# Kernel tuning notes

Measured on AMD Instinct MI355X. Metric: run time of the kernel, lower is better.

The kernel has to match this reference:

```python
import jax, jax.numpy as jnp
from jax import lax
import numpy as np

B, T, D, H, O = 256, 512, 512, 1024, 512

def setup_inputs() -> dict:
    key = jax.random.key(0)
    k1, k2, k3, k4 = jax.random.split(key, 4)
    return {
        "x": jax.random.normal(k1, (B, T, D), dtype=jnp.float32),
        "h0": jnp.zeros((B, H), dtype=jnp.float32),
        "w_xh": jax.random.normal(k2, (D, H), dtype=jnp.float32) * 0.05,
        "w_hh": jax.random.normal(k3, (H, H), dtype=jnp.float32) * 0.05,
        "w_hy": jax.random.normal(k4, (H, O), dtype=jnp.float32) * 0.05,
    }

def reference(x, h0, w_xh, w_hh, w_hy):
    # x: [B, T, D] -> scan over time. Each step matches MyRNNCell.call:
    #   h' = tanh(x_t @ W_xh + h @ W_hh);  y_t = h' @ W_hy
    xT = jnp.swapaxes(x, 0, 1)  # [T, B, D]
    def step(h, xt):
        h_next = jnp.tanh(xt @ w_xh + h @ w_hh)  # [B, H]
        return h_next, h_next @ w_hy             # output [B, O]
    h_final, outs = lax.scan(step, h0, xT)
    return jnp.swapaxes(outs, 0, 1), h_final  # [B, T, O], [B, H]
```

## Files before the change

kernel.cpp:

```cpp
#include <hip/hip_runtime.h>
#include <hip/hip_bf16.h>

#define BB 256
#define TT 512
#define DD 512
#define HH 1024
#define OO 512

typedef unsigned short u16;
typedef unsigned int u32;
typedef unsigned long long u64;
typedef __attribute__((ext_vector_type(8))) short frag8;
typedef __attribute__((ext_vector_type(4))) float floatx4;

#define MFMA16 __builtin_amdgcn_mfma_f32_16x16x32_bf16

__device__ __forceinline__ u16 f2b(float f) {
  union { float f; u32 u; } v; v.f = f;
  u32 r = v.u + 0x7fffu + ((v.u >> 16) & 1u);
  return (u16)(r >> 16);
}
__device__ __forceinline__ float b2f(u16 b) {
  union { u32 u; float f; } v; v.u = ((u32)b) << 16; return v.f;
}
__device__ __forceinline__ float fast_tanh(float x) {
  float e = __expf(2.0f * x);
  return 1.0f - 2.0f / (e + 1.0f);
}
__device__ __forceinline__ frag8 mkfrag(u64 lo, u64 hi) {
  union { u64 d[2]; frag8 f; } u; u.d[0] = lo; u.d[1] = hi; return u.f;
}

__global__ void k_transpose(const float* __restrict__ src, u16* __restrict__ dst,
                            int K, int N) {
  int idx = blockIdx.x * 256 + threadIdx.x;
  if (idx >= K * N) return;
  int k = idx / N, n = idx - k * N;
  dst[(u64)n * K + k] = f2b(src[idx]);
}

__global__ void k_init_s0(const float* __restrict__ h0, u16* __restrict__ S) {
  int idx = blockIdx.x * 256 + threadIdx.x;
  if (idx < BB * HH) S[idx] = f2b(h0[idx]);
}

__global__ void k_final_h(const u16* __restrict__ Sl, float* __restrict__ out) {
  int idx = blockIdx.x * 256 + threadIdx.x;
  if (idx < BB * HH) out[idx] = b2f(Sl[idx]);
}

__global__ void k_zero_flags(int* __restrict__ flags, int n) {
  int idx = blockIdx.x * 256 + threadIdx.x;
  if (idx < n) flags[idx] = 0;
}

__global__ __launch_bounds__(256) void k_gemm_xh(const float* __restrict__ X,
                                                 const u16* __restrict__ Wt,
                                                 u16* __restrict__ S) {
  __shared__ __align__(16) u16 As[64 * 72];
  __shared__ __align__(16) u16 Bs[64 * 72];
  const int tid = threadIdx.x;
  const int m0 = blockIdx.x * 64, n0 = blockIdx.y * 64;
  const int lane = tid & 63, wv = tid >> 6;
  const int fr = lane & 15, quad = lane >> 4;

  floatx4 acc[4];
#pragma unroll
  for (int i = 0; i < 4; ++i) acc[i] = (floatx4){0.f, 0.f, 0.f, 0.f};

  for (int kc = 0; kc < DD; kc += 64) {
    const float* Ab = X + (u64)m0 * DD + kc;
#pragma unroll
    for (int it = 0; it < 4; ++it) {
      int linear = (it * 256 + tid) * 4;
      int r = linear >> 6, c = linear & 63;
      float4 v = *(const float4*)(Ab + (u64)r * DD + c);
      ushort4 o;
      o.x = f2b(v.x); o.y = f2b(v.y); o.z = f2b(v.z); o.w = f2b(v.w);
      *(ushort4*)&As[r * 72 + c] = o;
    }
    const u16* Bb = Wt + (u64)n0 * DD + kc;
#pragma unroll
    for (int it = 0; it < 2; ++it) {
      int linear = (it * 256 + tid) * 8;
      int n = linear >> 6, c = linear & 63;
      *(uint4*)&Bs[n * 72 + c] = *(const uint4*)(Bb + (u64)n * DD + c);
    }
    __syncthreads();
#pragma unroll
    for (int kk = 0; kk < 64; kk += 32) {
      frag8 bf = *(const frag8*)&Bs[(wv * 16 + fr) * 72 + kk + quad * 8];
#pragma unroll
      for (int i = 0; i < 4; ++i) {
        frag8 af = *(const frag8*)&As[(i * 16 + fr) * 72 + kk + quad * 8];
        acc[i] = MFMA16(af, bf, acc[i], 0, 0, 0);
      }
    }
    __syncthreads();
  }
  const int col = n0 + wv * 16 + fr;
#pragma unroll
  for (int i = 0; i < 4; ++i) {
#pragma unroll
    for (int r = 0; r < 4; ++r) {
      int m = m0 + i * 16 + quad * 4 + r;
      int t = m & (TT - 1);
      int b = m >> 9;
      S[((u64)(t + 1) * BB + b) * HH + col] = f2b(acc[i][r]);
    }
  }
}

__global__ __launch_bounds__(256) void k_scan(const u16* __restrict__ Whh_t,
                                              u16* __restrict__ S,
                                              int* __restrict__ flags) {
  extern __shared__ __align__(16) u16 smem[];
  u16* Ws = smem;
  float* Red = (float*)(smem + 32 * 1032);

  const int tid = threadIdx.x;
  const int mb = blockIdx.x;
  const int nb = blockIdx.y;
  const int m0 = mb * 32, n0 = nb * 32;
  const int lane = tid & 63, wv = tid >> 6;
  const int fr = lane & 15, q = lane >> 4;
  const int kbase = wv * 256;
  const int er = tid >> 4;
  const int ec = (tid & 15) * 2;

  {
    const u16* Wb = Whh_t + (u64)n0 * HH;
#pragma unroll
    for (int it = 0; it < 16; ++it) {
      int linear = (it * 256 + tid) * 8;
      int r = linear >> 10, c = linear & 1023;
      *(uint4*)&Ws[r * 1032 + c] = *(const uint4*)(Wb + (u64)r * HH + c);
    }
  }
  __syncthreads();

  for (int t = 0; t < TT; ++t) {
    u16* Sout = S + (u64)(t + 1) * BB * HH + (u64)m0 * HH + n0;

    u32 z01 = *(const u32*)(Sout + (u64)er * HH + ec);
    u32 z23 = *(const u32*)(Sout + (u64)(er + 16) * HH + ec);
    asm volatile("" :: "v"(z01), "v"(z23));

    if (t > 0) {
      int* fb = flags + ((u64)(t - 1) * 8 + mb) * 32;
      if (lane < 8) {
        while (__hip_atomic_load(&fb[wv * 8 + lane], __ATOMIC_RELAXED,
                                 __HIP_MEMORY_SCOPE_AGENT) == 0) {
          __builtin_amdgcn_s_sleep(2);
        }
      }
      __builtin_amdgcn_fence(__ATOMIC_ACQUIRE, "workgroup");
    }

    const u16* St = S + (u64)t * BB * HH;
    const u64* A0p = (const u64*)(St + (u64)(m0 + fr) * HH + kbase + q * 8);
    const u64* A1p = (const u64*)(St + (u64)(m0 + 16 + fr) * HH + kbase + q * 8);
    u64 a0[16], a1[16];
#pragma unroll
    for (int kt = 0; kt < 8; ++kt) {
      a0[2 * kt]     = __hip_atomic_load(A0p + kt * 8,     __ATOMIC_RELAXED, __HIP_MEMORY_SCOPE_AGENT);
      a0[2 * kt + 1] = __hip_atomic_load(A0p + kt * 8 + 1, __ATOMIC_RELAXED, __HIP_MEMORY_SCOPE_AGENT);
      a1[2 * kt]     = __hip_atomic_load(A1p + kt * 8,     __ATOMIC_RELAXED, __HIP_MEMORY_SCOPE_AGENT);
      a1[2 * kt + 1] = __hip_atomic_load(A1p + kt * 8 + 1, __ATOMIC_RELAXED, __HIP_MEMORY_SCOPE_AGENT);
    }

    floatx4 acc[2][2];
#pragma unroll
    for (int i = 0; i < 2; ++i)
#pragma unroll
      for (int j = 0; j < 2; ++j) acc[i][j] = (floatx4){0.f, 0.f, 0.f, 0.f};

#pragma unroll
    for (int kt = 0; kt < 8; ++kt) {
      const int k = kbase + kt * 32 + q * 8;
      frag8 b0 = *(const frag8*)&Ws[fr * 1032 + k];
      frag8 b1 = *(const frag8*)&Ws[(16 + fr) * 1032 + k];
      frag8 af0 = mkfrag(a0[2 * kt], a0[2 * kt + 1]);
      frag8 af1 = mkfrag(a1[2 * kt], a1[2 * kt + 1]);
      acc[0][0] = MFMA16(af0, b0, acc[0][0], 0, 0, 0);
      acc[0][1] = MFMA16(af0, b1, acc[0][1], 0, 0, 0);
      acc[1][0] = MFMA16(af1, b0, acc[1][0], 0, 0, 0);
      acc[1][1] = MFMA16(af1, b1, acc[1][1], 0, 0, 0);
    }

#pragma unroll
    for (int im = 0; im < 2; ++im)
#pragma unroll
      for (int in = 0; in < 2; ++in)
#pragma unroll
        for (int r = 0; r < 4; ++r) {
          int row = im * 16 + q * 4 + r;
          int col = in * 16 + fr;
          Red[((u64)wv * 32 + row) * 33 + col] = acc[im][in][r];
        }
    __syncthreads();

    float s00 = Red[(0 * 32 + er) * 33 + ec]     + Red[(1 * 32 + er) * 33 + ec] +
                Red[(2 * 32 + er) * 33 + ec]     + Red[(3 * 32 + er) * 33 + ec];
    float s01 = Red[(0 * 32 + er) * 33 + ec + 1] + Red[(1 * 32 + er) * 33 + ec + 1] +
                Red[(2 * 32 + er) * 33 + ec + 1] + Red[(3 * 32 + er) * 33 + ec + 1];
    float s10 = Red[(0 * 32 + er + 16) * 33 + ec]     + Red[(1 * 32 + er + 16) * 33 + ec] +
                Red[(2 * 32 + er + 16) * 33 + ec]     + Red[(3 * 32 + er + 16) * 33 + ec];
    float s11 = Red[(0 * 32 + er + 16) * 33 + ec + 1] + Red[(1 * 32 + er + 16) * 33 + ec + 1] +
                Red[(2 * 32 + er + 16) * 33 + ec + 1] + Red[(3 * 32 + er + 16) * 33 + ec + 1];
    float z0 = b2f((u16)(z01 & 0xffffu)), z1 = b2f((u16)(z01 >> 16));
    float z2 = b2f((u16)(z23 & 0xffffu)), z3 = b2f((u16)(z23 >> 16));
    u32 p0 = (u32)f2b(fast_tanh(s00 + z0)) | ((u32)f2b(fast_tanh(s01 + z1)) << 16);
    u32 p1 = (u32)f2b(fast_tanh(s10 + z2)) | ((u32)f2b(fast_tanh(s11 + z3)) << 16);
    __hip_atomic_store((u32*)(Sout + (u64)er * HH + ec), p0,
                       __ATOMIC_RELAXED, __HIP_MEMORY_SCOPE_AGENT);
    __hip_atomic_store((u32*)(Sout + (u64)(er + 16) * HH + ec), p1,
                       __ATOMIC_RELAXED, __HIP_MEMORY_SCOPE_AGENT);
    __syncthreads();

    if (tid == 0) {
      __hip_atomic_store(&flags[((u64)t * 8 + mb) * 32 + nb], 1,
                         __ATOMIC_RELAXED, __HIP_MEMORY_SCOPE_AGENT);
    }
  }
}

__global__ __launch_bounds__(256) void k_gemm_hy(const u16* __restrict__ Hs,
                                                 const u16* __restrict__ Wt,
                                                 float* __restrict__ out) {
  __shared__ __align__(16) u16 As[64 * 72];
  __shared__ __align__(16) u16 Bs[64 * 72];
  const int tid = threadIdx.x;
  const int m0 = blockIdx.x * 64, n0 = blockIdx.y * 64;
  const int lane = tid & 63, wv = tid >> 6;
  const int fr = lane & 15, quad = lane >> 4;

  floatx4 acc[4];
#pragma unroll
  for (int i = 0; i < 4; ++i) acc[i] = (floatx4){0.f, 0.f, 0.f, 0.f};

  for (int kc = 0; kc < HH; kc += 64) {
    const u16* Ab = Hs + (u64)m0 * HH + kc;
#pragma unroll
    for (int it = 0; it < 2; ++it) {
      int linear = (it * 256 + tid) * 8;
      int r = linear >> 6, c = linear & 63;
      *(uint4*)&As[r * 72 + c] = *(const uint4*)(Ab + (u64)r * HH + c);
    }
    const u16* Bb = Wt + (u64)n0 * HH + kc;
#pragma unroll
    for (int it = 0; it < 2; ++it) {
      int linear = (it * 256 + tid) * 8;
      int n = linear >> 6, c = linear & 63;
      *(uint4*)&Bs[n * 72 + c] = *(const uint4*)(Bb + (u64)n * HH + c);
    }
    __syncthreads();
#pragma unroll
    for (int kk = 0; kk < 64; kk += 32) {
      frag8 bf = *(const frag8*)&Bs[(wv * 16 + fr) * 72 + kk + quad * 8];
#pragma unroll
      for (int i = 0; i < 4; ++i) {
        frag8 af = *(const frag8*)&As[(i * 16 + fr) * 72 + kk + quad * 8];
        acc[i] = MFMA16(af, bf, acc[i], 0, 0, 0);
      }
    }
    __syncthreads();
  }
  const int col = n0 + wv * 16 + fr;
#pragma unroll
  for (int i = 0; i < 4; ++i) {
#pragma unroll
    for (int r = 0; r < 4; ++r) {
      int m = m0 + i * 16 + quad * 4 + r;
      int t = m >> 8;
      int b = m & (BB - 1);
      out[(u64)b * (TT * OO) + (u64)t * OO + col] = acc[i][r];
    }
  }
}

extern "C" void kernel_launch(void* const* d_in, const int* in_sizes, int n_in,
                              void* d_out, int out_size, void* d_ws, size_t ws_size,
                              hipStream_t stream) {
  (void)in_sizes; (void)n_in; (void)out_size; (void)ws_size;
  const float* x    = (const float*)d_in[0];
  const float* h0   = (const float*)d_in[1];
  const float* w_xh = (const float*)d_in[2];
  const float* w_hh = (const float*)d_in[3];
  const float* w_hy = (const float*)d_in[4];
  float* out = (float*)d_out;

  u16* S = (u16*)d_ws;
  u64 s_elems = (u64)(TT + 1) * BB * HH;
  u16* Wxh_t = S + s_elems;
  u16* Whh_t = Wxh_t + (u64)HH * DD;
  u16* Why_t = Whh_t + (u64)HH * HH;
  int* flags = (int*)Wxh_t;
  const int n_flags = TT * 8 * 32;

  k_transpose<<<dim3((DD * HH + 255) / 256), dim3(256), 0, stream>>>(w_xh, Wxh_t, DD, HH);
  k_transpose<<<dim3((HH * HH + 255) / 256), dim3(256), 0, stream>>>(w_hh, Whh_t, HH, HH);
  k_transpose<<<dim3((HH * OO + 255) / 256), dim3(256), 0, stream>>>(w_hy, Why_t, HH, OO);
  k_init_s0<<<dim3(BB * HH / 256), dim3(256), 0, stream>>>(h0, S);

  k_gemm_xh<<<dim3((BB * TT) / 64, HH / 64), dim3(256), 0, stream>>>(x, Wxh_t, S);

  k_zero_flags<<<dim3((n_flags + 255) / 256), dim3(256), 0, stream>>>(flags, n_flags);

  const int scan_lds = 32 * 1032 * 2 + 4 * 32 * 33 * 4;
  hipFuncSetAttribute((const void*)k_scan,
                      hipFuncAttributeMaxDynamicSharedMemorySize, scan_lds);
  k_scan<<<dim3(8, 32), dim3(256), scan_lds, stream>>>(Whh_t, S, flags);

  k_gemm_hy<<<dim3((TT * BB) / 64, OO / 64), dim3(256), 0, stream>>>(
      S + (u64)BB * HH, Why_t, out);
  k_final_h<<<dim3(BB * HH / 256), dim3(256), 0, stream>>>(
      S + (u64)TT * BB * HH, out + (u64)BB * TT * OO);
}
```

Baseline: 3.964 ms.

## Fuse input projection into scan and replace flags with sentinel-value polling

Removes the separate x@W_xh GEMM and computes each step's input projection inside the persistent scan kernel, with W_xh slices held in LDS, so the xh projection no longer round-trips through the state buffer. The per-block flag array, its zeroing kernel and the second barrier are replaced by filling the state buffer with an all-ones sentinel and spinning on the data itself until no sentinel words remain. The reduction buffer is double-buffered to drop the trailing syncthreads, and packed bf16 conversion is used. This adds more LDS use and per-step reads of x inside the serial loop, and relies on a tanh output never encoding as the 0xFFFF sentinel pattern.

```diff
diff --git a/kernel.cpp b/kernel.cpp
--- a/kernel.cpp
+++ b/kernel.cpp
@@ -14,6 +14,8 @@
 typedef __attribute__((ext_vector_type(4))) float floatx4;
 
 #define MFMA16 __builtin_amdgcn_mfma_f32_16x16x32_bf16
+#define AL(p) __hip_atomic_load((p), __ATOMIC_RELAXED, __HIP_MEMORY_SCOPE_AGENT)
+#define AS(p, v) __hip_atomic_store((p), (v), __ATOMIC_RELAXED, __HIP_MEMORY_SCOPE_AGENT)
 
 __device__ __forceinline__ u16 f2b(float f) {
   union { float f; u32 u; } v; v.f = f;
@@ -29,6 +31,17 @@
 }
 __device__ __forceinline__ frag8 mkfrag(u64 lo, u64 hi) {
   union { u64 d[2]; frag8 f; } u; u.d[0] = lo; u.d[1] = hi; return u.f;
+}
+__device__ __forceinline__ u32 cvtpk(float lo, float hi) {
+  u32 r;
+  asm("v_cvt_pk_bf16_f32 %0, %1, %2" : "=v"(r) : "v"(lo), "v"(hi));
+  return r;
+}
+__device__ __forceinline__ frag8 cvt8(float4 a, float4 b) {
+  union { u32 w[4]; frag8 f; } u;
+  u.w[0] = cvtpk(a.x, a.y); u.w[1] = cvtpk(a.z, a.w);
+  u.w[2] = cvtpk(b.x, b.y); u.w[3] = cvtpk(b.z, b.w);
+  return u.f;
 }
 
 __global__ void k_transpose(const float* __restrict__ src, u16* __restrict__ dst,
@@ -49,74 +62,19 @@
   if (idx < BB * HH) out[idx] = b2f(Sl[idx]);
 }
 
-__global__ void k_zero_flags(int* __restrict__ flags, int n) {
-  int idx = blockIdx.x * 256 + threadIdx.x;
-  if (idx < n) flags[idx] = 0;
-}
-
-__global__ __launch_bounds__(256) void k_gemm_xh(const float* __restrict__ X,
-                                                 const u16* __restrict__ Wt,
-                                                 u16* __restrict__ S) {
-  __shared__ __align__(16) u16 As[64 * 72];
-  __shared__ __align__(16) u16 Bs[64 * 72];
-  const int tid = threadIdx.x;
-  const int m0 = blockIdx.x * 64, n0 = blockIdx.y * 64;
-  const int lane = tid & 63, wv = tid >> 6;
-  const int fr = lane & 15, quad = lane >> 4;
-
-  floatx4 acc[4];
-#pragma unroll
-  for (int i = 0; i < 4; ++i) acc[i] = (floatx4){0.f, 0.f, 0.f, 0.f};
-
-  for (int kc = 0; kc < DD; kc += 64) {
-    const float* Ab = X + (u64)m0 * DD + kc;
-#pragma unroll
-    for (int it = 0; it < 4; ++it) {
-      int linear = (it * 256 + tid) * 4;
-      int r = linear >> 6, c = linear & 63;
-      float4 v = *(const float4*)(Ab + (u64)r * DD + c);
-      ushort4 o;
-      o.x = f2b(v.x); o.y = f2b(v.y); o.z = f2b(v.z); o.w = f2b(v.w);
-      *(ushort4*)&As[r * 72 + c] = o;
-    }
-    const u16* Bb = Wt + (u64)n0 * DD + kc;
-#pragma unroll
-    for (int it = 0; it < 2; ++it) {
-      int linear = (it * 256 + tid) * 8;
-      int n = linear >> 6, c = linear & 63;
-      *(uint4*)&Bs[n * 72 + c] = *(const uint4*)(Bb + (u64)n * DD + c);
-    }
-    __syncthreads();
-#pragma unroll
-    for (int kk = 0; kk < 64; kk += 32) {
-      frag8 bf = *(const frag8*)&Bs[(wv * 16 + fr) * 72 + kk + quad * 8];
-#pragma unroll
-      for (int i = 0; i < 4; ++i) {
-        frag8 af = *(const frag8*)&As[(i * 16 + fr) * 72 + kk + quad * 8];
-        acc[i] = MFMA16(af, bf, acc[i], 0, 0, 0);
-      }
-    }
-    __syncthreads();
-  }
-  const int col = n0 + wv * 16 + fr;
-#pragma unroll
-  for (int i = 0; i < 4; ++i) {
-#pragma unroll
-    for (int r = 0; r < 4; ++r) {
-      int m = m0 + i * 16 + quad * 4 + r;
-      int t = m & (TT - 1);
-      int b = m >> 9;
-      S[((u64)(t + 1) * BB + b) * HH + col] = f2b(acc[i][r]);
-    }
-  }
+__global__ void k_fill_sent(uint4* __restrict__ p) {
+  u64 i = (u64)blockIdx.x * 256 + threadIdx.x;
+  p[i] = make_uint4(0xFFFFFFFFu, 0xFFFFFFFFu, 0xFFFFFFFFu, 0xFFFFFFFFu);
 }
 
 __global__ __launch_bounds__(256) void k_scan(const u16* __restrict__ Whh_t,
-                                              u16* __restrict__ S,
-                                              int* __restrict__ flags) {
+                                              const u16* __restrict__ Wxh_t,
+                                              const float* __restrict__ X,
+                                              u16* __restrict__ S) {
   extern __shared__ __align__(16) u16 smem[];
   u16* Ws = smem;
-  float* Red = (float*)(smem + 32 * 1032);
+  u16* Wxs = smem + 32 * 1032;
+  float* Red = (float*)(smem + 32 * 1032 + 32 * 520);
 
   const int tid = threadIdx.x;
   const int mb = blockIdx.x;
@@ -125,6 +83,7 @@
   const int lane = tid & 63, wv = tid >> 6;
   const int fr = lane & 15, q = lane >> 4;
   const int kbase = wv * 256;
+  const int xkbase = wv * 128;
   const int er = tid >> 4;
   const int ec = (tid & 15) * 2;
 
@@ -137,57 +96,75 @@
       *(uint4*)&Ws[r * 1032 + c] = *(const uint4*)(Wb + (u64)r * HH + c);
     }
   }
+  {
+    const u16* Wb = Wxh_t + (u64)n0 * DD;
+#pragma unroll
+    for (int it = 0; it < 8; ++it) {
+      int linear = (it * 256 + tid) * 8;
+      int r = linear >> 9, c = linear & 511;
+      *(uint4*)&Wxs[r * 520 + c] = *(const uint4*)(Wb + (u64)r * DD + c);
+    }
+  }
   __syncthreads();
 
   for (int t = 0; t < TT; ++t) {
-    u16* Sout = S + (u64)(t + 1) * BB * HH + (u64)m0 * HH + n0;
-
-    u32 z01 = *(const u32*)(Sout + (u64)er * HH + ec);
-    u32 z23 = *(const u32*)(Sout + (u64)(er + 16) * HH + ec);
-    asm volatile("" :: "v"(z01), "v"(z23));
-
-    if (t > 0) {
-      int* fb = flags + ((u64)(t - 1) * 8 + mb) * 32;
-      if (lane < 8) {
-        while (__hip_atomic_load(&fb[wv * 8 + lane], __ATOMIC_RELAXED,
-                                 __HIP_MEMORY_SCOPE_AGENT) == 0) {
-          __builtin_amdgcn_s_sleep(2);
-        }
-      }
-      __builtin_amdgcn_fence(__ATOMIC_ACQUIRE, "workgroup");
+    const float* xr0 = X + ((u64)(m0 + fr) * TT + t) * DD + xkbase;
+    const float* xr1 = X + ((u64)(m0 + 16 + fr) * TT + t) * DD + xkbase;
+    float4 xv[16];
+#pragma unroll
+    for (int xkt = 0; xkt < 4; ++xkt) {
+      xv[xkt * 4 + 0] = *(const float4*)(xr0 + xkt * 32 + q * 8);
+      xv[xkt * 4 + 1] = *(const float4*)(xr0 + xkt * 32 + q * 8 + 4);
+      xv[xkt * 4 + 2] = *(const float4*)(xr1 + xkt * 32 + q * 8);
+      xv[xkt * 4 + 3] = *(const float4*)(xr1 + xkt * 32 + q * 8 + 4);
+    }
+
+    floatx4 acc[2][2];
+#pragma unroll
+    for (int i = 0; i < 2; ++i)
+#pragma unroll
+      for (int j = 0; j < 2; ++j) acc[i][j] = (floatx4){0.f, 0.f, 0.f, 0.f};
+
+#pragma unroll
+    for (int xkt = 0; xkt < 4; ++xkt) {
+      const int k = xkbase + xkt * 32 + q * 8;
+      frag8 ax0 = cvt8(xv[xkt * 4 + 0], xv[xkt * 4 + 1]);
+      frag8 ax1 = cvt8(xv[xkt * 4 + 2], xv[xkt * 4 + 3]);
+      frag8 b0 = *(const frag8*)&Wxs[fr * 520 + k];
+      frag8 b1 = *(const frag8*)&Wxs[(16 + fr) * 520 + k];
+      acc[0][0] = MFMA16(ax0, b0, acc[0][0], 0, 0, 0);
+      acc[0][1] = MFMA16(ax0, b1, acc[0][1], 0, 0, 0);
+      acc[1][0] = MFMA16(ax1, b0, acc[1][0], 0, 0, 0);
+      acc[1][1] = MFMA16(ax1, b1, acc[1][1], 0, 0, 0);
     }
 
     const u16* St = S + (u64)t * BB * HH;
     const u64* A0p = (const u64*)(St + (u64)(m0 + fr) * HH + kbase + q * 8);
     const u64* A1p = (const u64*)(St + (u64)(m0 + 16 + fr) * HH + kbase + q * 8);
-    u64 a0[16], a1[16];
 #pragma unroll
     for (int kt = 0; kt < 8; ++kt) {
-      a0[2 * kt]     = __hip_atomic_load(A0p + kt * 8,     __ATOMIC_RELAXED, __HIP_MEMORY_SCOPE_AGENT);
-      a0[2 * kt + 1] = __hip_atomic_load(A0p + kt * 8 + 1, __ATOMIC_RELAXED, __HIP_MEMORY_SCOPE_AGENT);
-      a1[2 * kt]     = __hip_atomic_load(A1p + kt * 8,     __ATOMIC_RELAXED, __HIP_MEMORY_SCOPE_AGENT);
-      a1[2 * kt + 1] = __hip_atomic_load(A1p + kt * 8 + 1, __ATOMIC_RELAXED, __HIP_MEMORY_SCOPE_AGENT);
-    }
-
-    floatx4 acc[2][2];
-#pragma unroll
-    for (int i = 0; i < 2; ++i)
-#pragma unroll
-      for (int j = 0; j < 2; ++j) acc[i][j] = (floatx4){0.f, 0.f, 0.f, 0.f};
-
-#pragma unroll
-    for (int kt = 0; kt < 8; ++kt) {
+      u64 c0, c1, c2, c3;
+      for (;;) {
+        c0 = AL(A0p + kt * 8);     c1 = AL(A0p + kt * 8 + 1);
+        c2 = AL(A1p + kt * 8);     c3 = AL(A1p + kt * 8 + 1);
+        u32 bad = ((u32)c0 == 0xFFFFFFFFu) | ((u32)(c0 >> 32) == 0xFFFFFFFFu) |
+                  ((u32)c1 == 0xFFFFFFFFu) | ((u32)(c1 >> 32) == 0xFFFFFFFFu) |
+                  ((u32)c2 == 0xFFFFFFFFu) | ((u32)(c2 >> 32) == 0xFFFFFFFFu) |
+                  ((u32)c3 == 0xFFFFFFFFu) | ((u32)(c3 >> 32) == 0xFFFFFFFFu);
+        if (!bad) break;
+      }
       const int k = kbase + kt * 32 + q * 8;
       frag8 b0 = *(const frag8*)&Ws[fr * 1032 + k];
       frag8 b1 = *(const frag8*)&Ws[(16 + fr) * 1032 + k];
-      frag8 af0 = mkfrag(a0[2 * kt], a0[2 * kt + 1]);
-      frag8 af1 = mkfrag(a1[2 * kt], a1[2 * kt + 1]);
+      frag8 af0 = mkfrag(c0, c1);
+      frag8 af1 = mkfrag(c2, c3);
       acc[0][0] = MFMA16(af0, b0, acc[0][0], 0, 0, 0);
       acc[0][1] = MFMA16(af0, b1, acc[0][1], 0, 0, 0);
       acc[1][0] = MFMA16(af1, b0, acc[1][0], 0, 0, 0);
       acc[1][1] = MFMA16(af1, b1, acc[1][1], 0, 0, 0);
     }
 
+    float* R = Red + (t & 1) * (4 * 32 * 33);
 #pragma unroll
     for (int im = 0; im < 2; ++im)
 #pragma unroll
@@ -196,32 +173,23 @@
         for (int r = 0; r < 4; ++r) {
           int row = im * 16 + q * 4 + r;
           int col = in * 16 + fr;
-          Red[((u64)wv * 32 + row) * 33 + col] = acc[im][in][r];
+          R[(wv * 32 + row) * 33 + col] = acc[im][in][r];
         }
     __syncthreads();
 
-    float s00 = Red[(0 * 32 + er) * 33 + ec]     + Red[(1 * 32 + er) * 33 + ec] +
-                Red[(2 * 32 + er) * 33 + ec]     + Red[(3 * 32 + er) * 33 + ec];
-    float s01 = Red[(0 * 32 + er) * 33 + ec + 1] + Red[(1 * 32 + er) * 33 + ec + 1] +
-                Red[(2 * 32 + er) * 33 + ec + 1] + Red[(3 * 32 + er) * 33 + ec + 1];
-    float s10 = Red[(0 * 32 + er + 16) * 33 + ec]     + Red[(1 * 32 + er + 16) * 33 + ec] +
-                Red[(2 * 32 + er + 16) * 33 + ec]     + Red[(3 * 32 + er + 16) * 33 + ec];
-    float s11 = Red[(0 * 32 + er + 16) * 33 + ec + 1] + Red[(1 * 32 + er + 16) * 33 + ec + 1] +
-                Red[(2 * 32 + er + 16) * 33 + ec + 1] + Red[(3 * 32 + er + 16) * 33 + ec + 1];
-    float z0 = b2f((u16)(z01 & 0xffffu)), z1 = b2f((u16)(z01 >> 16));
-    float z2 = b2f((u16)(z23 & 0xffffu)), z3 = b2f((u16)(z23 >> 16));
-    u32 p0 = (u32)f2b(fast_tanh(s00 + z0)) | ((u32)f2b(fast_tanh(s01 + z1)) << 16);
-    u32 p1 = (u32)f2b(fast_tanh(s10 + z2)) | ((u32)f2b(fast_tanh(s11 + z3)) << 16);
-    __hip_atomic_store((u32*)(Sout + (u64)er * HH + ec), p0,
-                       __ATOMIC_RELAXED, __HIP_MEMORY_SCOPE_AGENT);
-    __hip_atomic_store((u32*)(Sout + (u64)(er + 16) * HH + ec), p1,
-                       __ATOMIC_RELAXED, __HIP_MEMORY_SCOPE_AGENT);
-    __syncthreads();
-
-    if (tid == 0) {
-      __hip_atomic_store(&flags[((u64)t * 8 + mb) * 32 + nb], 1,
-                         __ATOMIC_RELAXED, __HIP_MEMORY_SCOPE_AGENT);
-    }
+    u16* Sout = S + (u64)(t + 1) * BB * HH + (u64)m0 * HH + n0;
+    float s00 = R[(0 * 32 + er) * 33 + ec]     + R[(1 * 32 + er) * 33 + ec] +
+                R[(2 * 32 + er) * 33 + ec]     + R[(3 * 32 + er) * 33 + ec];
+    float s01 = R[(0 * 32 + er) * 33 + ec + 1] + R[(1 * 32 + er) * 33 + ec + 1] +
+                R[(2 * 32 + er) * 33 + ec + 1] + R[(3 * 32 + er) * 33 + ec + 1];
+    float s10 = R[(0 * 32 + er + 16) * 33 + ec]     + R[(1 * 32 + er + 16) * 33 + ec] +
+                R[(2 * 32 + er + 16) * 33 + ec]     + R[(3 * 32 + er + 16) * 33 + ec];
+    float s11 = R[(0 * 32 + er + 16) * 33 + ec + 1] + R[(1 * 32 + er + 16) * 33 + ec + 1] +
+                R[(2 * 32 + er + 16) * 33 + ec + 1] + R[(3 * 32 + er + 16) * 33 + ec + 1];
+    u32 p0 = cvtpk(fast_tanh(s00), fast_tanh(s01));
+    u32 p1 = cvtpk(fast_tanh(s10), fast_tanh(s11));
+    AS((u32*)(Sout + (u64)er * HH + ec), p0);
+    AS((u32*)(Sout + (u64)(er + 16) * HH + ec), p1);
   }
 }
 
@@ -295,22 +263,19 @@
   u16* Wxh_t = S + s_elems;
   u16* Whh_t = Wxh_t + (u64)HH * DD;
   u16* Why_t = Whh_t + (u64)HH * HH;
-  int* flags = (int*)Wxh_t;
-  const int n_flags = TT * 8 * 32;
 
   k_transpose<<<dim3((DD * HH + 255) / 256), dim3(256), 0, stream>>>(w_xh, Wxh_t, DD, HH);
   k_transpose<<<dim3((HH * HH + 255) / 256), dim3(256), 0, stream>>>(w_hh, Whh_t, HH, HH);
   k_transpose<<<dim3((HH * OO + 255) / 256), dim3(256), 0, stream>>>(w_hy, Why_t, HH, OO);
   k_init_s0<<<dim3(BB * HH / 256), dim3(256), 0, stream>>>(h0, S);
 
-  k_gemm_xh<<<dim3((BB * TT) / 64, HH / 64), dim3(256), 0, stream>>>(x, Wxh_t, S);
-
-  k_zero_flags<<<dim3((n_flags + 255) / 256), dim3(256), 0, stream>>>(flags, n_flags);
-
-  const int scan_lds = 32 * 1032 * 2 + 4 * 32 * 33 * 4;
+  k_fill_sent<<<dim3(65536), dim3(256), 0, stream>>>(
+      (uint4*)(S + (u64)BB * HH));
+
+  const int scan_lds = 32 * 1032 * 2 + 32 * 520 * 2 + 2 * 4 * 32 * 33 * 4;
   hipFuncSetAttribute((const void*)k_scan,
                       hipFuncAttributeMaxDynamicSharedMemorySize, scan_lds);
-  k_scan<<<dim3(8, 32), dim3(256), scan_lds, stream>>>(Whh_t, S, flags);
+  k_scan<<<dim3(8, 32), dim3(256), scan_lds, stream>>>(Whh_t, Wxh_t, x, S);
 
   k_gemm_hy<<<dim3((TT * BB) / 64, OO / 64), dim3(256), 0, stream>>>(
       S + (u64)BB * HH, Why_t, out);
```

Measured after the change: 4.060 ms. 1.02x slower.
